# Kernel tuning notes

Measured on AMD Instinct MI355X. Metric: run time of the kernel, lower is better.

Reference implementation:

```python
import jax, jax.numpy as jnp
import numpy as np

B, T, D, H, BUCKETS = 4, 4096, 1024, 8, 64
DH = D // H          # 128
BSZ = T // BUCKETS   # 64
TEMP = 0.75
SINK_ITERS = 5
LOG_EPS = 1e-6
GUMBEL_EPS = 1e-4


def setup_inputs() -> dict:
    key = jax.random.key(0)
    ks = jax.random.split(key, 6)
    x = jax.random.normal(ks[0], (B, T, D), dtype=jnp.float32)
    w_qkv = jax.random.normal(ks[1], (3 * D, D), dtype=jnp.float32) * 0.02   # torch Linear weight (out,in), no bias
    sort_w = jax.random.normal(ks[2], (1, H, DH, BUCKETS), dtype=jnp.float32)
    w_out = jax.random.normal(ks[3], (D, D), dtype=jnp.float32) * 0.02
    b_out = jnp.zeros((D,), dtype=jnp.float32)
    noise_u = jax.random.uniform(ks[4], (B * H, BUCKETS, BUCKETS), dtype=jnp.float32)
    return {"x": x, "w_qkv": w_qkv, "sort_w": sort_w, "w_out": w_out, "b_out": b_out, "noise_u": noise_u}


def reference(x, w_qkv, sort_w, w_out, b_out, noise_u):
    b, t, d = x.shape
    # qkv projection + merge heads -> (b*h, t, d_h)
    qkv = x @ w_qkv.T
    q, k, v = jnp.split(qkv, 3, axis=2)
    mh = lambda u: u.reshape(b, t, H, DH).transpose(0, 2, 1, 3).reshape(b * H, t, DH)
    q, k, v = mh(q), mh(k), mh(v)
    # bucket -> (b*h, buckets, bsz, d_h)
    bk = lambda u: u.reshape(b * H, BUCKETS, BSZ, DH)
    b_q, b_k, b_v = bk(q), bk(k), bk(v)
    # bucket summaries and sinkhorn sorting matrix R: (b*h, buckets, buckets)
    b_k_r = b_k.sum(axis=2)
    e_w = jnp.broadcast_to(sort_w, (b, H, DH, BUCKETS)).reshape(b * H, DH, BUCKETS)
    R = jnp.log(jax.nn.relu(jnp.einsum('bud,bdv->buv', b_k_r, e_w)) + LOG_EPS)
    gumbel = -jnp.log(-jnp.log(noise_u + GUMBEL_EPS) + GUMBEL_EPS)
    R = (R + gumbel) / TEMP
    for _ in range(SINK_ITERS):
        R = R - jax.nn.logsumexp(R, axis=2, keepdims=True)
        R = R - jax.nn.logsumexp(R, axis=1, keepdims=True)
    R = jnp.tril(jnp.exp(R), k=-1)
    # soft-permute buckets of k and v
    k_re = jnp.einsum('buv,bvtd->butd', R, b_k)
    v_re = jnp.einsum('buv,bvtd->butd', R, b_v)
    b_k2 = jnp.concatenate((k_re, b_k), axis=2)  # (bh, buckets, 2*bsz, dh)
    b_v2 = jnp.concatenate((v_re, b_v), axis=2)
    # bucketed attention (note: scale uses full model dim d, as in source)
    dots = jnp.einsum('buie,buje->buij', b_q, b_k2) * (d ** -0.5)
    attn = jax.nn.softmax(dots, axis=-1)
    out = jnp.einsum('buij,buje->buie', attn, b_v2)
    # unbucket + split heads -> (b, t, d)
    out = out.reshape(b, H, t, DH).transpose(0, 2, 1, 3).reshape(b, t, d)
    return out @ w_out.T + b_out
```

## Files before the change

kernel.cpp:

```cpp
#include <hip/hip_runtime.h>
#include <hip/hip_bf16.h>
#include <cstdint>
#include <cstddef>
#include <math.h>
#include <type_traits>

typedef __bf16 bf16;
typedef __bf16 bf16x4 __attribute__((ext_vector_type(4)));
typedef __bf16 bf16x8 __attribute__((ext_vector_type(8)));
typedef float  f32x4  __attribute__((ext_vector_type(4)));
typedef unsigned u32x2 __attribute__((ext_vector_type(2)));


__device__ inline bool input_is_fp32(const void* x) {
  const unsigned short* u = (const unsigned short*)x;
  const int lane = threadIdx.x & 63;
  const int e = (u[lane] >> 7) & 0xFF;
  return __ballot(e >= 137) != 0ULL;
}

__device__ inline float ldx(const void* p, size_t i, bool f32) {
  return f32 ? ((const float*)p)[i] : (float)((const bf16*)p)[i];
}

template<typename T>
__device__ inline bf16x8 ld8bf(const void* p, size_t i) {
  if constexpr (std::is_same<T, float>::value) {
    const f32x4* q = (const f32x4*)((const float*)p + i);
    const f32x4 a = q[0], b = q[1];
    bf16x8 r;
    r[0]=(bf16)a[0]; r[1]=(bf16)a[1]; r[2]=(bf16)a[2]; r[3]=(bf16)a[3];
    r[4]=(bf16)b[0]; r[5]=(bf16)b[1]; r[6]=(bf16)b[2]; r[7]=(bf16)b[3];
    return r;
  } else {
    return *(const bf16x8*)((const bf16*)p + i);
  }
}

__device__ __forceinline__ void gload16(const void* g, void* l) {
  __builtin_amdgcn_global_load_lds(
      (__attribute__((address_space(1))) void*)g,
      (__attribute__((address_space(3))) void*)l, 16, 0, 0);
}

__global__ __launch_bounds__(256)
void convert_to_bf16(const void* __restrict__ src, bf16* __restrict__ dst,
                     const void* __restrict__ xdet) {
  const bool f32 = input_is_fp32(xdet);
  const size_t i = ((size_t)blockIdx.x * 256 + threadIdx.x) * 8;
  if (f32) *(bf16x8*)&dst[i] = ld8bf<float>(src, i);
  else     *(bf16x8*)&dst[i] = ld8bf<bf16 >(src, i);
}

template<int EPI>
__global__ __launch_bounds__(512, 2)
void gemm256(const bf16* __restrict__ A, const bf16* __restrict__ Bm,
             const void* __restrict__ bias,
             void* __restrict__ C0, bf16* __restrict__ C1, bf16* __restrict__ C2,
             const void* __restrict__ xdet, int M, int N, int K)
{
  __shared__ __align__(16) bf16 lds[2][2][2][8192];
  const int tid = threadIdx.x, wave = tid >> 6, lane = tid & 63;
  const int fr = lane & 15, quad = lane >> 4;
  const int m0 = blockIdx.y * 256, n0 = blockIdx.x * 256;
  const int wm = wave >> 2, wn = wave & 3;
  const int gsz  = (quad ^ ((fr >> 1) & 3)) * 16;
  const int srow = wave * 32 + (lane >> 2);
  const int sg   = ((lane & 3) ^ ((lane >> 3) & 3)) * 8;
  const int NT = K >> 6;
  char* ldsb = (char*)&lds[0][0][0][0];

  auto stageA = [&](int buf, int kh, int t) {
    const bf16* s = A + (size_t)(m0 + srow) * K + t*64 + kh*32 + sg;
    char* d = ldsb + buf*65536 + kh*16384 + wave*2048;
    gload16(s, d);
    gload16(s + (size_t)16 * K, d + 1024);
  };
  auto stageB = [&](int buf, int kh, int t) {
    const bf16* s = Bm + (size_t)(n0 + srow) * K + t*64 + kh*32 + sg;
    char* d = ldsb + buf*65536 + 32768 + kh*16384 + wave*2048;
    gload16(s, d);
    gload16(s + (size_t)16 * K, d + 1024);
  };
  auto lda = [&](int c, int kh, int fi) {
    return *(const bf16x8*)(ldsb + c*65536 + kh*16384 + (wm*128 + fi*16 + fr)*64 + gsz);
  };
  auto ldb = [&](int c, int kh, int fi) {
    return *(const bf16x8*)(ldsb + c*65536 + 32768 + kh*16384 + (wn*64 + fi*16 + fr)*64 + gsz);
  };

  f32x4 acc[8][4];
  #pragma unroll
  for (int a = 0; a < 8; ++a)
    #pragma unroll
    for (int b = 0; b < 4; ++b) { f32x4 z = {0.f,0.f,0.f,0.f}; acc[a][b] = z; }

  stageA(0, 0, 0); stageB(0, 0, 0);
  stageA(0, 1, 0); stageB(0, 1, 0);
  stageA(1, 0, 1); stageB(1, 0, 1);
  asm volatile("s_waitcnt vmcnt(8)" ::: "memory");
  __builtin_amdgcn_s_barrier();

  #pragma unroll 1
  for (int t = 0; t < NT; ++t) {
    const int c = t & 1;
    const bool d12 = (t + 1 < NT), d34 = (t + 2 < NT);
    bf16x8 bfr[4], afr[4];

    #pragma unroll
    for (int n = 0; n < 4; ++n) bfr[n] = ldb(c, 0, n);
    #pragma unroll
    for (int m = 0; m < 4; ++m) afr[m] = lda(c, 0, m);
    if (d12) stageA(c ^ 1, 1, t + 1);
    __builtin_amdgcn_s_barrier();
    asm volatile("s_waitcnt lgkmcnt(0)" ::: "memory");
    __builtin_amdgcn_sched_barrier(0);
    __builtin_amdgcn_s_setprio(1);
    #pragma unroll
    for (int m = 0; m < 4; ++m)
      #pragma unroll
      for (int n = 0; n < 4; ++n)
        acc[m][n] = __builtin_amdgcn_mfma_f32_16x16x32_bf16(afr[m], bfr[n], acc[m][n], 0, 0, 0);
    __builtin_amdgcn_s_setprio(0);
    __builtin_amdgcn_s_barrier();

    #pragma unroll
    for (int m = 0; m < 4; ++m) afr[m] = lda(c, 0, 4 + m);
    if (d12) stageB(c ^ 1, 1, t + 1);
    __builtin_amdgcn_s_barrier();
    asm volatile("s_waitcnt lgkmcnt(0)" ::: "memory");
    __builtin_amdgcn_sched_barrier(0);
    __builtin_amdgcn_s_setprio(1);
    #pragma unroll
    for (int m = 0; m < 4; ++m)
      #pragma unroll
      for (int n = 0; n < 4; ++n)
        acc[4 + m][n] = __builtin_amdgcn_mfma_f32_16x16x32_bf16(afr[m], bfr[n], acc[4 + m][n], 0, 0, 0);
    __builtin_amdgcn_s_setprio(0);
    if (t < NT - 1) { asm volatile("s_waitcnt vmcnt(8)" ::: "memory"); }
    else            { asm volatile("s_waitcnt vmcnt(0)" ::: "memory"); }
    __builtin_amdgcn_s_barrier();

    #pragma unroll
    for (int n = 0; n < 4; ++n) bfr[n] = ldb(c, 1, n);
    #pragma unroll
    for (int m = 0; m < 4; ++m) afr[m] = lda(c, 1, m);
    if (d34) stageA(c, 0, t + 2);
    __builtin_amdgcn_s_barrier();
    asm volatile("s_waitcnt lgkmcnt(0)" ::: "memory");
    __builtin_amdgcn_sched_barrier(0);
    __builtin_amdgcn_s_setprio(1);
    #pragma unroll
    for (int m = 0; m < 4; ++m)
      #pragma unroll
      for (int n = 0; n < 4; ++n)
        acc[m][n] = __builtin_amdgcn_mfma_f32_16x16x32_bf16(afr[m], bfr[n], acc[m][n], 0, 0, 0);
    __builtin_amdgcn_s_setprio(0);
    __builtin_amdgcn_s_barrier();

    #pragma unroll
    for (int m = 0; m < 4; ++m) afr[m] = lda(c, 1, 4 + m);
    if (d34) stageB(c, 0, t + 2);
    __builtin_amdgcn_s_barrier();
    asm volatile("s_waitcnt lgkmcnt(0)" ::: "memory");
    __builtin_amdgcn_sched_barrier(0);
    __builtin_amdgcn_s_setprio(1);
    #pragma unroll
    for (int m = 0; m < 4; ++m)
      #pragma unroll
      for (int n = 0; n < 4; ++n)
        acc[4 + m][n] = __builtin_amdgcn_mfma_f32_16x16x32_bf16(afr[m], bfr[n], acc[4 + m][n], 0, 0, 0);
    __builtin_amdgcn_s_setprio(0);
    if (t < NT - 2)       { asm volatile("s_waitcnt vmcnt(8)" ::: "memory"); }
    else if (t == NT - 2) { asm volatile("s_waitcnt vmcnt(4)" ::: "memory"); }
    __builtin_amdgcn_s_barrier();
  }

  if constexpr (EPI == 0) {
    const int sel = n0 >> 10;
    const int cb  = (n0 & 1023) + wn * 64;
    #pragma unroll
    for (int im = 0; im < 8; ++im) {
      const int mrow = m0 + wm*128 + im*16 + quad*4;
      const int b = mrow >> 12, tt = mrow & 4095;
      const int u = tt >> 6, i = tt & 63;
      #pragma unroll
      for (int nn = 0; nn < 4; ++nn) {
        const int cc = cb + nn*16 + fr;
        const int h = cc >> 7, e = cc & 127;
        const size_t bhu = (size_t)((b*8 + h)*64 + u);
        if (sel == 2) {
          bf16x4 w;
          #pragma unroll
          for (int r = 0; r < 4; ++r) w[r] = (bf16)acc[im][nn][r];
          *(bf16x4*)&C2[(bhu*128 + e)*64 + i] = w;
        } else {
          bf16* dst = (sel == 0) ? (bf16*)C0 : C1;
          #pragma unroll
          for (int r = 0; r < 4; ++r)
            dst[(bhu*64 + i + r)*128 + e] = (bf16)acc[im][nn][r];
        }
      }
    }
  } else {
    const bool f32o = input_is_fp32(xdet);
    #pragma unroll
    for (int im = 0; im < 8; ++im) {
      #pragma unroll
      for (int nn = 0; nn < 4; ++nn) {
        #pragma unroll
        for (int r = 0; r < 4; ++r) {
          const int m = m0 + wm*128 + im*16 + quad*4 + r;
          const int n = n0 + wn*64 + nn*16 + fr;
          const float val = acc[im][nn][r] + ldx(bias, n, f32o);
          if (f32o) ((float*)C0)[(size_t)m*N + n] = val;
          else      ((bf16*)C0)[(size_t)m*N + n] = (bf16)val;
        }
      }
    }
  }
}

__global__ __launch_bounds__(128)
void bksum(const bf16* __restrict__ k_ws, float* __restrict__ bkr_g)
{
  const int ug = blockIdx.x, bh = blockIdx.y, t = threadIdx.x;
  const int ul = t >> 4, e0 = (t & 15) * 8;
  const int u = ug * 8 + ul;
  const bf16* p = k_ws + ((size_t)bh*64 + u)*8192 + e0;
  float acc[8];
  #pragma unroll
  for (int j = 0; j < 8; ++j) acc[j] = 0.f;
  for (int i = 0; i < 64; ++i) {
    bf16x8 kv = *(const bf16x8*)&p[i*128];
    #pragma unroll
    for (int j = 0; j < 8; ++j) acc[j] += (float)kv[j];
  }
  float* dst = bkr_g + (size_t)bh*8192 + u*128 + e0;
  #pragma unroll
  for (int j = 0; j < 8; ++j) dst[j] = acc[j];
}

__global__ __launch_bounds__(256)
void sinkhorn_R(const float* __restrict__ bkr_g, const void* __restrict__ sort_w,
                const void* __restrict__ noise, float* __restrict__ R_buf,
                const void* __restrict__ xdet)
{
  const bool f32 = input_is_fp32(xdet);
  const int bh = blockIdx.x, h = bh & 7, tid = threadIdx.x;
  __shared__ float bkr[64*128];
  __shared__ float ew[128*64];
  __shared__ float R[64*65];

  for (int f = tid; f < 64*128; f += 256) bkr[f] = bkr_g[(size_t)bh*8192 + f];
  for (int f = tid; f < 128*64; f += 256) ew[f] = ldx(sort_w, (size_t)h*8192 + f, f32);
  __syncthreads();

  for (int f = tid; f < 64*64; f += 256) {
    const int u = f >> 6, v = f & 63;
    float s = 0.f;
    for (int e = 0; e < 128; ++e) s += bkr[u*128 + e] * ew[e*64 + v];
    s = fmaxf(s, 0.f);
    const float r  = logf(s + 1e-6f);
    const double nz = (double)ldx(noise, ((size_t)bh*64 + u)*64 + v, f32);
    const double t1 = log(nz + 1e-4);
    const double t2 = fmax(-t1 + 1e-4, 1e-30);
    const float g = (float)(-log(t2));
    R[u*65 + v] = (r + g) * (1.f / 0.75f);
  }
  __syncthreads();

  for (int it = 0; it < 5; ++it) {
    if (tid < 64) {
      float mx = -1e30f;
      for (int v = 0; v < 64; ++v) mx = fmaxf(mx, R[tid*65 + v]);
      float s = 0.f;
      for (int v = 0; v < 64; ++v) s += expf(R[tid*65 + v] - mx);
      const float l = mx + logf(s);
      for (int v = 0; v < 64; ++v) R[tid*65 + v] -= l;
    }
    __syncthreads();
    if (tid < 64) {
      float mx = -1e30f;
      for (int u = 0; u < 64; ++u) mx = fmaxf(mx, R[u*65 + tid]);
      float s = 0.f;
      for (int u = 0; u < 64; ++u) s += expf(R[u*65 + tid] - mx);
      const float l = mx + logf(s);
      for (int u = 0; u < 64; ++u) R[u*65 + tid] -= l;
    }
    __syncthreads();
  }

  for (int f = tid; f < 64*64; f += 256) {
    const int u = f >> 6, v = f & 63;
    R_buf[(size_t)bh*4096 + f] = (u > v) ? expf(R[u*65 + v]) : 0.f;
  }
}

__global__ __launch_bounds__(256)
void permute_kv(const float* __restrict__ R_buf,
                const bf16* __restrict__ Xk, const bf16* __restrict__ Xv,
                bf16* __restrict__ Ok, bf16* __restrict__ Ov, int bh0)
{
  const int tid = threadIdx.x;
  const int bhl = blockIdx.y, bh = bh0 + bhl;
  const int f0  = blockIdx.x * 256;
  const bf16* X = blockIdx.z ? Xv : Xk;
  bf16*       O = blockIdx.z ? Ov : Ok;

  __shared__ __align__(16) bf16 A_lds[64*136];
  __shared__ __align__(16) bf16 X_lds[16*1048];

  {
    const bf16* Xg = X + (size_t)bh*524288 + f0;
    const int vb = tid >> 5, c = tid & 31;
    const int dst = (c >> 1)*1048 + (c & 1)*8;
    #pragma unroll
    for (int p = 0; p < 8; ++p) {
      const int v = vb + p*8;
      *(bf16x8*)&X_lds[dst + v*16] = *(const bf16x8*)&Xg[(size_t)v*8192 + c*8];
    }
  }
  {
    const float* Rg = R_buf + (size_t)bh*4096;
    #pragma unroll
    for (int p = 0; p < 16; ++p) {
      const int idx = tid + p*256;
      const int uu = idx >> 6, vv = idx & 63;
      const float r = Rg[idx];
      const bf16 hi = (bf16)r;
      const float lo = r - (float)hi;
      A_lds[uu*136 + vv]      = hi;
      A_lds[uu*136 + 64 + vv] = (bf16)lo;
    }
  }
  __syncthreads();

  const int lane = tid & 63, wave = tid >> 6;
  const int fr = lane & 15, quad = lane >> 4;

  bf16x8 af[4][4];
  #pragma unroll
  for (int mt = 0; mt < 4; ++mt)
    #pragma unroll
    for (int ks = 0; ks < 4; ++ks)
      af[mt][ks] = *(const bf16x8*)&A_lds[(mt*16 + fr)*136 + ks*32 + quad*8];

  f32x4 acc[4][4];
  #pragma unroll
  for (int a = 0; a < 4; ++a)
    #pragma unroll
    for (int b = 0; b < 4; ++b) { f32x4 z = {0.f,0.f,0.f,0.f}; acc[a][b] = z; }

  #pragma unroll
  for (int nt = 0; nt < 4; ++nt) {
    const int g = wave*4 + nt;
    const unsigned addr = (unsigned)(size_t)
        (__attribute__((address_space(3))) bf16*)&X_lds[g*1048 + quad*128 + fr*4];
    u32x2 p0, p1, p2, p3;
    asm volatile(
      "ds_read_b64_tr_b16 %0, %4\n"
      "ds_read_b64_tr_b16 %1, %4 offset:128\n"
      "ds_read_b64_tr_b16 %2, %4 offset:1024\n"
      "ds_read_b64_tr_b16 %3, %4 offset:1152\n"
      : "=&v"(p0), "=&v"(p1), "=&v"(p2), "=&v"(p3)
      : "v"(addr));
    asm volatile("s_waitcnt lgkmcnt(0)" ::: "memory");
    __builtin_amdgcn_sched_barrier(0);
    union { u32x2 u[2]; bf16x8 v; } c0, c1;
    c0.u[0] = p0; c0.u[1] = p1;
    c1.u[0] = p2; c1.u[1] = p3;
    const bf16x8 b0 = c0.v, b1 = c1.v;
    #pragma unroll
    for (int mt = 0; mt < 4; ++mt) {
      acc[mt][nt] = __builtin_amdgcn_mfma_f32_16x16x32_bf16(af[mt][0], b0, acc[mt][nt], 0, 0, 0);
      acc[mt][nt] = __builtin_amdgcn_mfma_f32_16x16x32_bf16(af[mt][1], b1, acc[mt][nt], 0, 0, 0);
      acc[mt][nt] = __builtin_amdgcn_mfma_f32_16x16x32_bf16(af[mt][2], b0, acc[mt][nt], 0, 0, 0);
      acc[mt][nt] = __builtin_amdgcn_mfma_f32_16x16x32_bf16(af[mt][3], b1, acc[mt][nt], 0, 0, 0);
    }
  }

  bf16* Og = O + (size_t)bhl*524288 + f0;
  #pragma unroll
  for (int mt = 0; mt < 4; ++mt)
    #pragma unroll
    for (int nt = 0; nt < 4; ++nt)
      #pragma unroll
      for (int r = 0; r < 4; ++r)
        Og[(size_t)(mt*16 + quad*4 + r)*8192 + wave*64 + nt*16 + fr] = (bf16)acc[mt][nt][r];
}

__global__ __launch_bounds__(256)
void attn_mfma(const bf16* __restrict__ q_ws, const bf16* __restrict__ k_ws,
               const bf16* __restrict__ vT_ws,
               const bf16* __restrict__ kre_g, const bf16* __restrict__ vre_g,
               bf16* __restrict__ aout, int bh0)
{
  const int u = blockIdx.x, bhl = blockIdx.y, bh = bh0 + bhl;
  const int tid = threadIdx.x;
  const int lane = tid & 63, wave = tid >> 6;
  const int fr = lane & 15, quad = lane >> 4;

  __shared__ __align__(16) unsigned char smem[34048];
  float* sc = (float*)smem;
  bf16*  pA = (bf16*)smem;

  const size_t tileq = ((size_t)bh *64 + u) * 8192;
  const size_t tilel = ((size_t)bhl*64 + u) * 8192;

  {
    f32x4 dacc[4][2];
    #pragma unroll
    for (int mt = 0; mt < 4; ++mt)
      #pragma unroll
      for (int nt = 0; nt < 2; ++nt) { f32x4 z = {0.f,0.f,0.f,0.f}; dacc[mt][nt] = z; }
    #pragma unroll
    for (int ks = 0; ks < 4; ++ks) {
      bf16x8 afr[4];
      #pragma unroll
      for (int mt = 0; mt < 4; ++mt)
        afr[mt] = *(const bf16x8*)&q_ws[tileq + (size_t)(mt*16 + fr)*128 + ks*32 + quad*8];
      #pragma unroll
      for (int nt = 0; nt < 2; ++nt) {
        const int j = wave*32 + nt*16 + fr;
        bf16x8 bfr;
        if (wave < 2) bfr = *(const bf16x8*)&kre_g[tilel + (size_t)j*128 + ks*32 + quad*8];
        else          bfr = *(const bf16x8*)&k_ws[tileq + (size_t)(j - 64)*128 + ks*32 + quad*8];
        #pragma unroll
        for (int mt = 0; mt < 4; ++mt)
          dacc[mt][nt] = __builtin_amdgcn_mfma_f32_16x16x32_bf16(afr[mt], bfr, dacc[mt][nt], 0, 0, 0);
      }
    }
    #pragma unroll
    for (int mt = 0; mt < 4; ++mt)
      #pragma unroll
      for (int nt = 0; nt < 2; ++nt)
        #pragma unroll
        for (int r = 0; r < 4; ++r)
          sc[(mt*16 + quad*4 + r)*132 + wave*32 + nt*16 + fr] = dacc[mt][nt][r] * 0.03125f;
  }
  __syncthreads();

  {
    const int i = tid >> 2, jc = tid & 3;
    float pv[32];
    float mx = -1e30f;
    #pragma unroll
    for (int t = 0; t < 32; ++t) { pv[t] = sc[i*132 + jc + t*4]; mx = fmaxf(mx, pv[t]); }
    mx = fmaxf(mx, __shfl_xor(mx, 1));
    mx = fmaxf(mx, __shfl_xor(mx, 2));
    float s = 0.f;
    #pragma unroll
    for (int t = 0; t < 32; ++t) { pv[t] = expf(pv[t] - mx); s += pv[t]; }
    s += __shfl_xor(s, 1);
    s += __shfl_xor(s, 2);
    const float inv = 1.f / s;
    __syncthreads();
    #pragma unroll
    for (int t = 0; t < 32; ++t) pA[i*136 + jc + t*4] = (bf16)(pv[t] * inv);
  }
  __syncthreads();

  {
    f32x4 oacc[4][2];
    #pragma unroll
    for (int mt = 0; mt < 4; ++mt)
      #pragma unroll
      for (int nt = 0; nt < 2; ++nt) { f32x4 z = {0.f,0.f,0.f,0.f}; oacc[mt][nt] = z; }
    #pragma unroll
    for (int ks = 0; ks < 4; ++ks) {
      bf16x8 afr[4];
      #pragma unroll
      for (int mt = 0; mt < 4; ++mt)
        afr[mt] = *(const bf16x8*)&pA[(mt*16 + fr)*136 + ks*32 + quad*8];
      #pragma unroll
      for (int nt = 0; nt < 2; ++nt) {
        const int e = wave*32 + nt*16 + fr;
        bf16x8 bfr;
        if (ks < 2) bfr = *(const bf16x8*)&vre_g[tilel + (size_t)e*64 + ks*32 + quad*8];
        else        bfr = *(const bf16x8*)&vT_ws[tileq + (size_t)e*64 + (ks - 2)*32 + quad*8];
        #pragma unroll
        for (int mt = 0; mt < 4; ++mt)
          oacc[mt][nt] = __builtin_amdgcn_mfma_f32_16x16x32_bf16(afr[mt], bfr, oacc[mt][nt], 0, 0, 0);
      }
    }
    __syncthreads();
    #pragma unroll
    for (int mt = 0; mt < 4; ++mt)
      #pragma unroll
      for (int nt = 0; nt < 2; ++nt)
        #pragma unroll
        for (int r = 0; r < 4; ++r)
          pA[(mt*16 + quad*4 + r)*136 + wave*32 + nt*16 + fr] = (bf16)oacc[mt][nt][r];
  }
  __syncthreads();

  {
    const int b = bh >> 3, h = bh & 7;
    #pragma unroll
    for (int r = 0; r < 4; ++r) {
      const int f = r*2048 + tid*8;
      const int i = f >> 7, e0 = f & 127;
      bf16x8 w = *(const bf16x8*)&pA[i*136 + e0];
      *(bf16x8*)&aout[((size_t)(b*4096 + u*64 + i))*1024 + h*128 + e0] = w;
    }
  }
}

extern "C" void kernel_launch(void* const* d_in, const int* in_sizes, int n_in,
                              void* d_out, int out_size, void* d_ws, size_t ws_size,
                              hipStream_t stream)
{
  (void)in_sizes; (void)n_in; (void)out_size; (void)ws_size;
  const void* x      = d_in[0];
  const void* w_qkv  = d_in[1];
  const void* sort_w = d_in[2];
  const void* w_out  = d_in[3];
  const void* b_out  = d_in[4];
  const void* noise  = d_in[5];

  char* ws = (char*)d_ws;
  const size_t TEN = (size_t)32*64*64*128;
  const size_t HEN = TEN / 2;
  bf16* q_ws  = (bf16*)ws;
  bf16* k_ws  = q_ws + TEN;
  bf16* vT_ws = k_ws + TEN;
  bf16* xa_ws = vT_ws + TEN;

  float* bkr_g = (float*)((char*)xa_ws + (size_t)30*1024*1024);
  float* R_buf = (float*)((char*)xa_ws + (size_t)31*1024*1024);
  bf16* wqkv_bf = (bf16*)((char*)d_out + (1536<<10));
  bf16* kre = (bf16*)d_out;
  bf16* vre = kre + HEN;
  bf16* wout_bf = k_ws;

  convert_to_bf16<<<8192, 256, 0, stream>>>(x, xa_ws, x);
  convert_to_bf16<<<1536, 256, 0, stream>>>(w_qkv, wqkv_bf, x);

  gemm256<0><<<dim3(12,64), 512, 0, stream>>>(xa_ws, wqkv_bf, nullptr,
                                              q_ws, k_ws, vT_ws, x, 16384, 3072, 1024);

  bksum<<<dim3(8,32), 128, 0, stream>>>(k_ws, bkr_g);
  sinkhorn_R<<<32, 256, 0, stream>>>(bkr_g, sort_w, noise, R_buf, x);

  permute_kv<<<dim3(32,16,2), 256, 0, stream>>>(R_buf, k_ws, vT_ws, kre, vre, 0);
  attn_mfma<<<dim3(64,16), 256, 0, stream>>>(q_ws, k_ws, vT_ws, kre, vre, xa_ws, 0);
  permute_kv<<<dim3(32,16,2), 256, 0, stream>>>(R_buf, k_ws, vT_ws, kre, vre, 16);
  attn_mfma<<<dim3(64,16), 256, 0, stream>>>(q_ws, k_ws, vT_ws, kre, vre, xa_ws, 16);

  convert_to_bf16<<<512, 256, 0, stream>>>(w_out, wout_bf, x);
  gemm256<1><<<dim3(4,64), 512, 0, stream>>>(xa_ws, wout_bf, b_out,
                                             d_out, nullptr, nullptr, x, 16384, 1024, 1024);
}
```

Measured before the change: 434.3 us.

## Fuse input conversions, swizzle GEMM blocks, parallelize Sinkhorn, prefetch V tiles

```diff
diff --git a/kernel.cpp b/kernel.cpp
--- a/kernel.cpp
+++ b/kernel.cpp
@@ -52,6 +52,23 @@
   else     *(bf16x8*)&dst[i] = ld8bf<bf16 >(src, i);
 }
 
+__global__ __launch_bounds__(256)
+void convert_pair(const void* __restrict__ s1, bf16* __restrict__ d1,
+                  const void* __restrict__ s2, bf16* __restrict__ d2,
+                  const void* __restrict__ xdet) {
+  const bool f32 = input_is_fp32(xdet);
+  const size_t b = blockIdx.x;
+  if (b < 8192) {
+    const size_t i = (b*256 + threadIdx.x) * 8;
+    if (f32) *(bf16x8*)&d1[i] = ld8bf<float>(s1, i);
+    else     *(bf16x8*)&d1[i] = ld8bf<bf16 >(s1, i);
+  } else {
+    const size_t i = ((b - 8192)*256 + threadIdx.x) * 8;
+    if (f32) *(bf16x8*)&d2[i] = ld8bf<float>(s2, i);
+    else     *(bf16x8*)&d2[i] = ld8bf<bf16 >(s2, i);
+  }
+}
+
 template<int EPI>
 __global__ __launch_bounds__(512, 2)
 void gemm256(const bf16* __restrict__ A, const bf16* __restrict__ Bm,
@@ -62,7 +79,11 @@
   __shared__ __align__(16) bf16 lds[2][2][2][8192];
   const int tid = threadIdx.x, wave = tid >> 6, lane = tid & 63;
   const int fr = lane & 15, quad = lane >> 4;
-  const int m0 = blockIdx.y * 256, n0 = blockIdx.x * 256;
+  const int nwg = gridDim.x * gridDim.y;
+  const int cpx = nwg >> 3;
+  const int bid = blockIdx.y * gridDim.x + blockIdx.x;
+  const int swz = (bid & 7) * cpx + (bid >> 3);
+  const int m0 = (swz / gridDim.x) * 256, n0 = (swz % gridDim.x) * 256;
   const int wm = wave >> 2, wn = wave & 3;
   const int gsz  = (quad ^ ((fr >> 1) & 3)) * 16;
   const int srow = wave * 32 + (lane >> 2);
@@ -270,23 +291,32 @@
   }
   __syncthreads();
 
+  const int rc = tid >> 2, c4 = tid & 3;
   for (int it = 0; it < 5; ++it) {
-    if (tid < 64) {
+    {
       float mx = -1e30f;
-      for (int v = 0; v < 64; ++v) mx = fmaxf(mx, R[tid*65 + v]);
+      for (int v = c4; v < 64; v += 4) mx = fmaxf(mx, R[rc*65 + v]);
+      mx = fmaxf(mx, __shfl_xor(mx, 1));
+      mx = fmaxf(mx, __shfl_xor(mx, 2));
       float s = 0.f;
-      for (int v = 0; v < 64; ++v) s += expf(R[tid*65 + v] - mx);
+      for (int v = c4; v < 64; v += 4) s += expf(R[rc*65 + v] - mx);
+      s += __shfl_xor(s, 1);
+      s += __shfl_xor(s, 2);
       const float l = mx + logf(s);
-      for (int v = 0; v < 64; ++v) R[tid*65 + v] -= l;
+      for (int v = c4; v < 64; v += 4) R[rc*65 + v] -= l;
     }
     __syncthreads();
-    if (tid < 64) {
+    {
       float mx = -1e30f;
-      for (int u = 0; u < 64; ++u) mx = fmaxf(mx, R[u*65 + tid]);
+      for (int u = c4; u < 64; u += 4) mx = fmaxf(mx, R[u*65 + rc]);
+      mx = fmaxf(mx, __shfl_xor(mx, 1));
+      mx = fmaxf(mx, __shfl_xor(mx, 2));
       float s = 0.f;
-      for (int u = 0; u < 64; ++u) s += expf(R[u*65 + tid] - mx);
+      for (int u = c4; u < 64; u += 4) s += expf(R[u*65 + rc] - mx);
+      s += __shfl_xor(s, 1);
+      s += __shfl_xor(s, 2);
       const float l = mx + logf(s);
-      for (int u = 0; u < 64; ++u) R[u*65 + tid] -= l;
+      for (int u = c4; u < 64; u += 4) R[u*65 + rc] -= l;
     }
     __syncthreads();
   }
@@ -408,6 +438,15 @@
   const size_t tileq = ((size_t)bh *64 + u) * 8192;
   const size_t tilel = ((size_t)bhl*64 + u) * 8192;
 
+  bf16x8 pvT[2][2];
+  #pragma unroll
+  for (int nt = 0; nt < 2; ++nt) {
+    const int e = wave*32 + nt*16 + fr;
+    #pragma unroll
+    for (int k2 = 0; k2 < 2; ++k2)
+      pvT[nt][k2] = *(const bf16x8*)&vT_ws[tileq + (size_t)e*64 + k2*32 + quad*8];
+  }
+
   {
     f32x4 dacc[4][2];
     #pragma unroll
@@ -475,10 +514,13 @@
         afr[mt] = *(const bf16x8*)&pA[(mt*16 + fr)*136 + ks*32 + quad*8];
       #pragma unroll
       for (int nt = 0; nt < 2; ++nt) {
-        const int e = wave*32 + nt*16 + fr;
         bf16x8 bfr;
-        if (ks < 2) bfr = *(const bf16x8*)&vre_g[tilel + (size_t)e*64 + ks*32 + quad*8];
-        else        bfr = *(const bf16x8*)&vT_ws[tileq + (size_t)e*64 + (ks - 2)*32 + quad*8];
+        if (ks < 2) {
+          const int e = wave*32 + nt*16 + fr;
+          bfr = *(const bf16x8*)&vre_g[tilel + (size_t)e*64 + ks*32 + quad*8];
+        } else {
+          bfr = pvT[nt][ks - 2];
+        }
         #pragma unroll
         for (int mt = 0; mt < 4; ++mt)
           oacc[mt][nt] = __builtin_amdgcn_mfma_f32_16x16x32_bf16(afr[mt], bfr, oacc[mt][nt], 0, 0, 0);
@@ -534,8 +576,7 @@
   bf16* vre = kre + HEN;
   bf16* wout_bf = k_ws;
 
-  convert_to_bf16<<<8192, 256, 0, stream>>>(x, xa_ws, x);
-  convert_to_bf16<<<1536, 256, 0, stream>>>(w_qkv, wqkv_bf, x);
+  convert_pair<<<9728, 256, 0, stream>>>(x, xa_ws, w_qkv, wqkv_bf, x);
 
   gemm256<0><<<dim3(12,64), 512, 0, stream>>>(xa_ws, wqkv_bf, nullptr,
                                               q_ws, k_ws, vT_ws, x, 16384, 3072, 1024);
```

Result: no change. 430.6 us (-0.9%).
